# Optimization experiments

Measured on AMD Instinct MI355X. Metric: run time of the kernel, lower is better.

Reference implementation:

```python
import jax, jax.numpy as jnp
import numpy as np

N_NODES = 100000
N_EDGES = 1600000
D = 64


def setup_inputs() -> dict:
    key = jax.random.key(0)
    ks = jax.random.split(key, 9)
    x = jax.random.normal(ks[0], (N_NODES, D), dtype=jnp.float32)
    src = jax.random.randint(ks[1], (N_EDGES,), 0, N_NODES, dtype=jnp.int64)
    dst = jax.random.randint(ks[2], (N_EDGES,), 0, N_NODES, dtype=jnp.int64)
    s = 1.0 / np.sqrt(D)
    W_self1 = jax.random.normal(ks[3], (D, D), dtype=jnp.float32) * s
    W_neigh1 = jax.random.normal(ks[4], (D, D), dtype=jnp.float32) * s
    b1 = jnp.zeros((D,), dtype=jnp.float32)
    W_self2 = jax.random.normal(ks[5], (D, D), dtype=jnp.float32) * s
    W_neigh2 = jax.random.normal(ks[6], (D, D), dtype=jnp.float32) * s
    b2 = jnp.zeros((D,), dtype=jnp.float32)
    return {"x": x, "src": src, "dst": dst,
            "W_self1": W_self1, "W_neigh1": W_neigh1, "b1": b1,
            "W_self2": W_self2, "W_neigh2": W_neigh2, "b2": b2}


def _sage_layer(h, src, dst, W_self, W_neigh, b, n_nodes):
    # gather source-node features along edges: [E, d]
    msg = h[src]
    # sum messages into destination nodes, then normalize by in-degree (mean agg)
    agg = jax.ops.segment_sum(msg, dst, num_segments=n_nodes)
    deg = jax.ops.segment_sum(jnp.ones((src.shape[0], 1), h.dtype), dst,
                              num_segments=n_nodes)
    h_neigh = agg / jnp.maximum(deg, 1.0)
    # DGL SAGEConv (mean): fc_self(h) + fc_neigh(h_neigh) + bias
    return h @ W_self + h_neigh @ W_neigh + b


def reference(x, src, dst, W_self1, W_neigh1, b1, W_self2, W_neigh2, b2):
    n = x.shape[0]
    h = _sage_layer(x, src, dst, W_self1, W_neigh1, b1, n)
    # note: source module's forward applies no activation between layers
    h = _sage_layer(h, src, dst, W_self2, W_neigh2, b2, n)
    return h
```

## Files before the change

kernel.cpp:

```cpp
#include <hip/hip_runtime.h>
#include <hip/hip_bf16.h>


#define D 64
#define CAP 64
#define BNODES 256
#define BCAP 4736
#define MAXNB 512
#define WT_STRIDE 144

typedef __bf16 bf16x8 __attribute__((ext_vector_type(8)));
typedef float  f32x4  __attribute__((ext_vector_type(4)));

__device__ __forceinline__ unsigned pack2(float a, float b) {
    __hip_bfloat162 t = __float22bfloat162_rn(make_float2(a, b));
    return *(unsigned*)&t;
}
__device__ __forceinline__ unsigned short f2b(float f) {
    __hip_bfloat16 b = __float2bfloat16(f);
    return *(unsigned short*)&b;
}


__global__ void __launch_bounds__(256)
prep_kernel(const float4* __restrict__ x, uint4* __restrict__ xb4,
            unsigned* __restrict__ xsent, unsigned* __restrict__ h1sent,
            int* __restrict__ esent,
            const int* __restrict__ src, const int* __restrict__ dst,
            int* __restrict__ gcur, int* __restrict__ gbucket,
            int E, int NB, int n8, int bin_blocks, int N) {
    const int bid = blockIdx.x;
    const int t   = threadIdx.x;

    if (bid < bin_blocks) {
        __shared__ int hist[MAXNB];
        for (int i = t; i < NB; i += 256) hist[i] = 0;
        __syncthreads();

        const int e4_total = E >> 2;
        const int base4    = bid * 1024;

        int4 sv[4], dv[4];
        bool have[4];
        #pragma unroll
        for (int k = 0; k < 4; ++k) {
            int i4 = base4 + t + k * 256;
            have[k] = i4 < e4_total;
            if (have[k]) {
                sv[k] = ((const int4*)src)[i4];
                dv[k] = ((const int4*)dst)[i4];
            }
        }

        #pragma unroll
        for (int k = 0; k < 4; ++k) if (have[k]) {
            atomicAdd(&hist[dv[k].x >> 8], 1);
            atomicAdd(&hist[dv[k].y >> 8], 1);
            atomicAdd(&hist[dv[k].z >> 8], 1);
            atomicAdd(&hist[dv[k].w >> 8], 1);
        }

        int  tail_s = 0, tail_d = 0;
        bool have_tail = false;
        if (bid == 0) {
            int e = (e4_total << 2) + t;
            if (e < E) {
                tail_s = src[e]; tail_d = dst[e]; have_tail = true;
                atomicAdd(&hist[tail_d >> 8], 1);
            }
        }
        __syncthreads();

        for (int i = t; i < NB; i += 256) {
            int c = hist[i];
            hist[i] = (c > 0) ? atomicAdd(&gcur[i], c) : 0;
        }
        __syncthreads();

        #pragma unroll
        for (int k = 0; k < 4; ++k) if (have[k]) {
            int4 s = sv[k], d = dv[k];
            int b, p;
            b = d.x >> 8; p = atomicAdd(&hist[b], 1); if (p < BCAP) gbucket[b * BCAP + p] = ((d.x & 255) << 17) | s.x;
            b = d.y >> 8; p = atomicAdd(&hist[b], 1); if (p < BCAP) gbucket[b * BCAP + p] = ((d.y & 255) << 17) | s.y;
            b = d.z >> 8; p = atomicAdd(&hist[b], 1); if (p < BCAP) gbucket[b * BCAP + p] = ((d.z & 255) << 17) | s.z;
            b = d.w >> 8; p = atomicAdd(&hist[b], 1); if (p < BCAP) gbucket[b * BCAP + p] = ((d.w & 255) << 17) | s.w;
        }
        if (have_tail) {
            int b = tail_d >> 8, p = atomicAdd(&hist[b], 1);
            if (p < BCAP) gbucket[b * BCAP + p] = ((tail_d & 255) << 17) | tail_s;
        }
        return;
    }

    const int cb = bid - bin_blocks;
    const int i  = cb * 256 + t;
    if (i < n8) {
        float4 a = x[2 * i], b = x[2 * i + 1];
        uint4 o;
        o.x = pack2(a.x, a.y);
        o.y = pack2(a.z, a.w);
        o.z = pack2(b.x, b.y);
        o.w = pack2(b.z, b.w);
        xb4[i] = o;
    }
    if (cb == 0) {
        if (t < 32)              xsent[t] = 0u;
        else if (t < 64)         h1sent[t - 32] = 0u;
        else if (t < 64 + CAP)   esent[t - 64] = N;
    }
}


__global__ void __launch_bounds__(256)
ellify_kernel(const int* __restrict__ gcur, const int* __restrict__ gbucket,
              int* __restrict__ cnt, int* __restrict__ edge_idx, int N) {
    __shared__ int scnt[BNODES];
    scnt[threadIdx.x] = 0;
    __syncthreads();

    const int b     = blockIdx.x;
    const int ne    = min(gcur[b], BCAP);
    const int node0 = b << 8;

    for (int e = threadIdx.x; e < ne; e += 256) {
        int p   = gbucket[b * BCAP + e];
        int s   = p & 0x1FFFF;
        int ld  = p >> 17;
        int pos = atomicAdd(&scnt[ld], 1);
        if (pos < CAP) edge_idx[(size_t)(node0 + ld) * CAP + pos] = s;
    }
    __syncthreads();

    int node = node0 + threadIdx.x;
    if (node < N) {
        int raw = scnt[threadIdx.x];
        cnt[node] = raw;
        int c  = min(raw, CAP);
        int c8 = (c + 7) & ~7;
        for (int p = c; p < c8; ++p)
            edge_idx[(size_t)node * CAP + p] = N;
    }
}


__device__ __forceinline__ void acc8(float& a0, float& a1, float& a2, float& a3,
                                     float& a4, float& a5, float& a6, float& a7,
                                     uint4 u) {
    a0 += __uint_as_float(u.x << 16);
    a1 += __uint_as_float(u.x & 0xffff0000u);
    a2 += __uint_as_float(u.y << 16);
    a3 += __uint_as_float(u.y & 0xffff0000u);
    a4 += __uint_as_float(u.z << 16);
    a5 += __uint_as_float(u.z & 0xffff0000u);
    a6 += __uint_as_float(u.w << 16);
    a7 += __uint_as_float(u.w & 0xffff0000u);
}

__device__ __forceinline__ bf16x8 asbf(uint4 u) {
    union { uint4 a; bf16x8 v; } c; c.a = u; return c.v;
}

__global__ void __launch_bounds__(256, 3)
fused_kernel(const unsigned short* __restrict__ h,
             const int* __restrict__ cnt,
             const int* __restrict__ edge_idx,
             const float* __restrict__ Wself,
             const float* __restrict__ Wneigh,
             const float* __restrict__ bias,
             float* __restrict__ out_f32,
             unsigned short* __restrict__ out_bf16, int N) {
    __shared__ __align__(16) unsigned short wt[64 * WT_STRIDE];

    {
        const int t    = threadIdx.x;
        const int krow = t >> 1;
        const int c0   = (t & 1) * 32;
        const float* Wrow = (krow < 64) ? (Wself + krow * 64)
                                        : (Wneigh + (krow - 64) * 64);
        for (int i = 0; i < 32; i += 4) {
            float4 w = *(const float4*)(Wrow + c0 + i);
            const int n0 = c0 + i;
            wt[(n0 + 0) * WT_STRIDE + krow] = f2b(w.x);
            wt[(n0 + 1) * WT_STRIDE + krow] = f2b(w.y);
            wt[(n0 + 2) * WT_STRIDE + krow] = f2b(w.z);
            wt[(n0 + 3) * WT_STRIDE + krow] = f2b(w.w);
        }
    }
    __syncthreads();

    const int lane = threadIdx.x & 63;
    const int q    = lane & 7;
    const int g    = lane >> 3;
    const int col  = lane & 15;
    const int quad = lane >> 4;
    const int wave = blockIdx.x * (blockDim.x >> 6) + (threadIdx.x >> 6);
    const int n_waves = gridDim.x * (blockDim.x >> 6);

    const int tiles = (N + 15) >> 4;
    int t = wave;
    if (t >= tiles) return;

    float bv[4];
    #pragma unroll
    for (int nt = 0; nt < 4; ++nt) bv[nt] = bias[nt * 16 + col];

    const uint4* __restrict__ h4 = (const uint4*)h;
    const int SENT = N * CAP;

    int pcA, pcB, psrA, psrB;
    {
        const int nodeA = t * 16 + g, nodeB = nodeA + 8;
        const int aA = (nodeA < N) ? nodeA : 0;
        const int aB = (nodeB < N) ? nodeB : 0;
        const int lA = cnt[aA], lB = cnt[aB];
        pcA  = (nodeA < N) ? lA : 0;
        pcB  = (nodeB < N) ? lB : 0;
        psrA = edge_idx[aA * CAP + q];
        psrB = edge_idx[aB * CAP + q];
    }

    for (; t < tiles; t += n_waves) {
        const int cA  = min(pcA, CAP), cB = min(pcB, CAP);
        const int c8A = (cA + 7) & ~7, c8B = (cB + 7) & ~7;
        const int nodeA  = t * 16 + g;
        const int startA = ((nodeA < N) ? nodeA : 0) * CAP;
        const int startB = ((nodeA + 8 < N) ? nodeA + 8 : 0) * CAP;
        const int cmax = max(c8A, c8B);
        const int b0   = g << 3;
        int srA = psrA, srB = psrB;

        {
            const int tn = t + n_waves;
            const int tc = (tn < tiles) ? tn : t;
            const int nA = tc * 16 + g, nB = nA + 8;
            const int aA = (nA < N) ? nA : 0;
            const int aB = (nB < N) ? nB : 0;
            const int lA = cnt[aA], lB = cnt[aB];
            pcA  = (nA < N) ? lA : 0;
            pcB  = (nB < N) ? lB : 0;
            psrA = edge_idx[aA * CAP + q];
            psrB = edge_idx[aB * CAP + q];
        }

        int row = t * 16 + col;
        if (row >= N) row = N - 1;
        uint4 A0u = h4[(size_t)row * 8 + quad];
        uint4 A1u = h4[(size_t)row * 8 + 4 + quad];

        float a0 = 0.f, a1 = 0.f, a2 = 0.f, a3 = 0.f;
        float a4 = 0.f, a5 = 0.f, a6 = 0.f, a7 = 0.f;
        float b0f = 0.f, b1f = 0.f, b2f = 0.f, b3f = 0.f;
        float b4f = 0.f, b5f = 0.f, b6f = 0.f, b7f = 0.f;

        for (int j = 0; j < cmax; j += 8) {
            const int jn = j + 8;
            const int srA_n = edge_idx[((jn < c8A) ? startA + jn : SENT) + q];
            const int srB_n = edge_idx[((jn < c8B) ? startB + jn : SENT) + q];

            const int sA0 = __shfl(srA, b0 + 0, 64);
            const int sA1 = __shfl(srA, b0 + 1, 64);
            const int sA2 = __shfl(srA, b0 + 2, 64);
            const int sA3 = __shfl(srA, b0 + 3, 64);
            const int sA4 = __shfl(srA, b0 + 4, 64);
            const int sA5 = __shfl(srA, b0 + 5, 64);
            const int sA6 = __shfl(srA, b0 + 6, 64);
            const int sA7 = __shfl(srA, b0 + 7, 64);
            const int sB0 = __shfl(srB, b0 + 0, 64);
            const int sB1 = __shfl(srB, b0 + 1, 64);
            const int sB2 = __shfl(srB, b0 + 2, 64);
            const int sB3 = __shfl(srB, b0 + 3, 64);
            const int sB4 = __shfl(srB, b0 + 4, 64);
            const int sB5 = __shfl(srB, b0 + 5, 64);
            const int sB6 = __shfl(srB, b0 + 6, 64);
            const int sB7 = __shfl(srB, b0 + 7, 64);

            uint4 uA0 = h4[(size_t)sA0 * 8 + q];
            uint4 uA1 = h4[(size_t)sA1 * 8 + q];
            uint4 uA2 = h4[(size_t)sA2 * 8 + q];
            uint4 uA3 = h4[(size_t)sA3 * 8 + q];
            uint4 uA4 = h4[(size_t)sA4 * 8 + q];
            uint4 uA5 = h4[(size_t)sA5 * 8 + q];
            uint4 uA6 = h4[(size_t)sA6 * 8 + q];
            uint4 uA7 = h4[(size_t)sA7 * 8 + q];
            uint4 uB0 = h4[(size_t)sB0 * 8 + q];
            uint4 uB1 = h4[(size_t)sB1 * 8 + q];
            uint4 uB2 = h4[(size_t)sB2 * 8 + q];
            uint4 uB3 = h4[(size_t)sB3 * 8 + q];
            uint4 uB4 = h4[(size_t)sB4 * 8 + q];
            uint4 uB5 = h4[(size_t)sB5 * 8 + q];
            uint4 uB6 = h4[(size_t)sB6 * 8 + q];
            uint4 uB7 = h4[(size_t)sB7 * 8 + q];

            __builtin_amdgcn_sched_barrier(0);

            acc8(a0, a1, a2, a3, a4, a5, a6, a7, uA0);
            acc8(a0, a1, a2, a3, a4, a5, a6, a7, uA1);
            acc8(a0, a1, a2, a3, a4, a5, a6, a7, uA2);
            acc8(a0, a1, a2, a3, a4, a5, a6, a7, uA3);
            acc8(a0, a1, a2, a3, a4, a5, a6, a7, uA4);
            acc8(a0, a1, a2, a3, a4, a5, a6, a7, uA5);
            acc8(a0, a1, a2, a3, a4, a5, a6, a7, uA6);
            acc8(a0, a1, a2, a3, a4, a5, a6, a7, uA7);
            acc8(b0f, b1f, b2f, b3f, b4f, b5f, b6f, b7f, uB0);
            acc8(b0f, b1f, b2f, b3f, b4f, b5f, b6f, b7f, uB1);
            acc8(b0f, b1f, b2f, b3f, b4f, b5f, b6f, b7f, uB2);
            acc8(b0f, b1f, b2f, b3f, b4f, b5f, b6f, b7f, uB3);
            acc8(b0f, b1f, b2f, b3f, b4f, b5f, b6f, b7f, uB4);
            acc8(b0f, b1f, b2f, b3f, b4f, b5f, b6f, b7f, uB5);
            acc8(b0f, b1f, b2f, b3f, b4f, b5f, b6f, b7f, uB6);
            acc8(b0f, b1f, b2f, b3f, b4f, b5f, b6f, b7f, uB7);

            srA = srA_n;
            srB = srB_n;
        }

        const float invA = (cA > 0) ? 1.0f / (float)cA : 0.0f;
        const float invB = (cB > 0) ? 1.0f / (float)cB : 0.0f;
        uint4 P0, P1;
        P0.x = pack2(a0 * invA, a1 * invA);
        P0.y = pack2(a2 * invA, a3 * invA);
        P0.z = pack2(a4 * invA, a5 * invA);
        P0.w = pack2(a6 * invA, a7 * invA);
        P1.x = pack2(b0f * invB, b1f * invB);
        P1.y = pack2(b2f * invB, b3f * invB);
        P1.z = pack2(b4f * invB, b5f * invB);
        P1.w = pack2(b6f * invB, b7f * invB);

        const int srcA2 = ((lane & 7) << 3) + quad;
        const int srcA3 = srcA2 + 4;
        const bool hi   = (lane & 8) != 0;
        uint4 A2u, A3u;
        {
            unsigned l0 = __shfl(P0.x, srcA2, 64), h0 = __shfl(P1.x, srcA2, 64);
            unsigned l1 = __shfl(P0.y, srcA2, 64), h1 = __shfl(P1.y, srcA2, 64);
            unsigned l2 = __shfl(P0.z, srcA2, 64), h2 = __shfl(P1.z, srcA2, 64);
            unsigned l3 = __shfl(P0.w, srcA2, 64), h3 = __shfl(P1.w, srcA2, 64);
            A2u.x = hi ? h0 : l0;  A2u.y = hi ? h1 : l1;
            A2u.z = hi ? h2 : l2;  A2u.w = hi ? h3 : l3;
        }
        {
            unsigned l0 = __shfl(P0.x, srcA3, 64), h0 = __shfl(P1.x, srcA3, 64);
            unsigned l1 = __shfl(P0.y, srcA3, 64), h1 = __shfl(P1.y, srcA3, 64);
            unsigned l2 = __shfl(P0.z, srcA3, 64), h2 = __shfl(P1.z, srcA3, 64);
            unsigned l3 = __shfl(P0.w, srcA3, 64), h3 = __shfl(P1.w, srcA3, 64);
            A3u.x = hi ? h0 : l0;  A3u.y = hi ? h1 : l1;
            A3u.z = hi ? h2 : l2;  A3u.w = hi ? h3 : l3;
        }

        bf16x8 A0 = asbf(A0u), A1 = asbf(A1u);
        bf16x8 A2 = asbf(A2u), A3 = asbf(A3u);

        __builtin_amdgcn_sched_barrier(0);
        int ob = 0;
        asm volatile("" : "+v"(ob));
        bf16x8 Bf[4][4];
        #pragma unroll
        for (int nt = 0; nt < 4; ++nt) {
            const int n = nt * 16 + col;
            #pragma unroll
            for (int kk = 0; kk < 4; ++kk) {
                const int kcat0 = ((kk >= 2) ? 64 : 0) + (kk & 1) * 32 + quad * 8;
                const char* p = (const char*)wt + n * (WT_STRIDE * 2) + kcat0 * 2 + ob;
                Bf[nt][kk] = *(const bf16x8*)p;
            }
        }

        #pragma unroll
        for (int nt = 0; nt < 4; ++nt) {
            f32x4 acc = {bv[nt], bv[nt], bv[nt], bv[nt]};
            acc = __builtin_amdgcn_mfma_f32_16x16x32_bf16(A0, Bf[nt][0], acc, 0, 0, 0);
            acc = __builtin_amdgcn_mfma_f32_16x16x32_bf16(A1, Bf[nt][1], acc, 0, 0, 0);
            acc = __builtin_amdgcn_mfma_f32_16x16x32_bf16(A2, Bf[nt][2], acc, 0, 0, 0);
            acc = __builtin_amdgcn_mfma_f32_16x16x32_bf16(A3, Bf[nt][3], acc, 0, 0, 0);
            if (out_f32) {
                #pragma unroll
                for (int r = 0; r < 4; ++r) {
                    const int orow = t * 16 + quad * 4 + r;
                    if (orow < N) out_f32[(size_t)orow * D + nt * 16 + col] = acc[r];
                }
            } else {
                #pragma unroll
                for (int r = 0; r < 4; ++r) {
                    const int orow = t * 16 + quad * 4 + r;
                    if (orow < N) out_bf16[(size_t)orow * D + nt * 16 + col] = f2b(acc[r]);
                }
            }
        }
    }
}


extern "C" void kernel_launch(void* const* d_in, const int* in_sizes, int n_in,
                              void* d_out, int out_size, void* d_ws, size_t ws_size,
                              hipStream_t stream) {
    const float* x   = (const float*)d_in[0];
    const int*   src = (const int*)d_in[1];
    const int*   dst = (const int*)d_in[2];
    const float* Ws1 = (const float*)d_in[3];
    const float* Wn1 = (const float*)d_in[4];
    const float* b1  = (const float*)d_in[5];
    const float* Ws2 = (const float*)d_in[6];
    const float* Wn2 = (const float*)d_in[7];
    const float* b2  = (const float*)d_in[8];

    const int N = in_sizes[0] / D;
    const int E = in_sizes[1];

    float* out = (float*)d_out;

    const int NB = (N + BNODES - 1) / BNODES;

    int* gcur      = (int*)d_ws;
    int* cnt       = gcur + 512;
    int* edge_idx  = cnt + N;
    unsigned short* xb   = (unsigned short*)(edge_idx + (size_t)(N + 1) * CAP);
    unsigned short* h1b  = xb + (size_t)(N + 1) * D;
    int* gbucket   = (int*)(h1b + (size_t)(N + 1) * D);

    const int n8         = N * D / 8;
    const int cvt_blocks = (n8 + 255) / 256;
    const int e4_total   = E >> 2;
    const int bin_blocks = (e4_total + 1023) / 1024 > 0 ? (e4_total + 1023) / 1024 : 1;

    hipMemsetAsync(gcur, 0, 512 * sizeof(int), stream);

    prep_kernel<<<bin_blocks + cvt_blocks, 256, 0, stream>>>(
        (const float4*)x, (uint4*)xb,
        (unsigned*)(xb + (size_t)N * D), (unsigned*)(h1b + (size_t)N * D),
        edge_idx + (size_t)N * CAP,
        src, dst, gcur, gbucket, E, NB, n8, bin_blocks, N);

    ellify_kernel<<<NB, 256, 0, stream>>>(gcur, gbucket, cnt, edge_idx, N);

    const int fblocks = 768;

    fused_kernel<<<fblocks, 256, 0, stream>>>(xb, cnt, edge_idx, Ws1, Wn1, b1,
                                              nullptr, h1b, N);
    fused_kernel<<<fblocks, 256, 0, stream>>>(h1b, cnt, edge_idx, Ws2, Wn2, b2,
                                              out, nullptr, N);
}
```

Measured before the change: 197.7 us.

## Sort edges locally in shared memory before coalesced global bucket and ELL writes

The binning kernel now computes a per-block prefix sum over bucket counts, counting-sorts its edges into shared memory, and then writes each bucket's entries to global memory as contiguous runs instead of scattering them individually. The ellify kernel likewise counting-sorts each bucket by local node in shared memory and writes full 64-entry ELL rows with vectorized int4 stores, padding with the sentinel. The aim is coalesced global writes in place of random 4-byte scatters. In exchange it adds serial single-thread prefix scans, more shared memory (which may lower occupancy), and extra barriers, and every row is now written in full.

```diff
diff --git a/kernel.cpp b/kernel.cpp
--- a/kernel.cpp
+++ b/kernel.cpp
@@ -33,8 +33,14 @@
     const int t   = threadIdx.x;
 
     if (bid < bin_blocks) {
-        __shared__ int hist[MAXNB];
-        for (int i = t; i < NB; i += 256) hist[i] = 0;
+        __shared__ int            bcnt[MAXNB];
+        __shared__ int            pofs[MAXNB];
+        __shared__ int            sofs[MAXNB];
+        __shared__ int            gbase[MAXNB];
+        __shared__ int            ssort[4096];
+        __shared__ unsigned short sbkt[4096];
+
+        for (int i = t; i < NB; i += 256) bcnt[i] = 0;
         __syncthreads();
 
         const int e4_total = E >> 2;
@@ -54,41 +60,53 @@
 
         #pragma unroll
         for (int k = 0; k < 4; ++k) if (have[k]) {
-            atomicAdd(&hist[dv[k].x >> 8], 1);
-            atomicAdd(&hist[dv[k].y >> 8], 1);
-            atomicAdd(&hist[dv[k].z >> 8], 1);
-            atomicAdd(&hist[dv[k].w >> 8], 1);
-        }
-
-        int  tail_s = 0, tail_d = 0;
-        bool have_tail = false;
+            atomicAdd(&bcnt[dv[k].x >> 8], 1);
+            atomicAdd(&bcnt[dv[k].y >> 8], 1);
+            atomicAdd(&bcnt[dv[k].z >> 8], 1);
+            atomicAdd(&bcnt[dv[k].w >> 8], 1);
+        }
+        __syncthreads();
+
+        if (t == 0) {
+            int acc = 0;
+            for (int i = 0; i < NB; ++i) { pofs[i] = acc; acc += bcnt[i]; }
+        }
+        __syncthreads();
+        for (int i = t; i < NB; i += 256) sofs[i] = pofs[i];
+        __syncthreads();
+
+        #pragma unroll
+        for (int k = 0; k < 4; ++k) if (have[k]) {
+            int4 s = sv[k], d = dv[k];
+            int b, p;
+            b = d.x >> 8; p = atomicAdd(&sofs[b], 1); ssort[p] = ((d.x & 255) << 17) | s.x; sbkt[p] = (unsigned short)b;
+            b = d.y >> 8; p = atomicAdd(&sofs[b], 1); ssort[p] = ((d.y & 255) << 17) | s.y; sbkt[p] = (unsigned short)b;
+            b = d.z >> 8; p = atomicAdd(&sofs[b], 1); ssort[p] = ((d.z & 255) << 17) | s.z; sbkt[p] = (unsigned short)b;
+            b = d.w >> 8; p = atomicAdd(&sofs[b], 1); ssort[p] = ((d.w & 255) << 17) | s.w; sbkt[p] = (unsigned short)b;
+        }
+        __syncthreads();
+
+        for (int i = t; i < NB; i += 256) {
+            int c = bcnt[i];
+            gbase[i] = (c > 0) ? atomicAdd(&gcur[i], c) : 0;
+        }
+        __syncthreads();
+
+        const int eblk = (min(base4 + 1024, e4_total) - base4) << 2;
+        for (int i = t; i < eblk; i += 256) {
+            const int b    = sbkt[i];
+            const int gpos = gbase[b] + (i - pofs[b]);
+            if (gpos < BCAP) gbucket[b * BCAP + gpos] = ssort[i];
+        }
+
         if (bid == 0) {
             int e = (e4_total << 2) + t;
             if (e < E) {
-                tail_s = src[e]; tail_d = dst[e]; have_tail = true;
-                atomicAdd(&hist[tail_d >> 8], 1);
+                int s = src[e], d = dst[e];
+                int b = d >> 8;
+                int p = atomicAdd(&gcur[b], 1);
+                if (p < BCAP) gbucket[b * BCAP + p] = ((d & 255) << 17) | s;
             }
-        }
-        __syncthreads();
-
-        for (int i = t; i < NB; i += 256) {
-            int c = hist[i];
-            hist[i] = (c > 0) ? atomicAdd(&gcur[i], c) : 0;
-        }
-        __syncthreads();
-
-        #pragma unroll
-        for (int k = 0; k < 4; ++k) if (have[k]) {
-            int4 s = sv[k], d = dv[k];
-            int b, p;
-            b = d.x >> 8; p = atomicAdd(&hist[b], 1); if (p < BCAP) gbucket[b * BCAP + p] = ((d.x & 255) << 17) | s.x;
-            b = d.y >> 8; p = atomicAdd(&hist[b], 1); if (p < BCAP) gbucket[b * BCAP + p] = ((d.y & 255) << 17) | s.y;
-            b = d.z >> 8; p = atomicAdd(&hist[b], 1); if (p < BCAP) gbucket[b * BCAP + p] = ((d.z & 255) << 17) | s.z;
-            b = d.w >> 8; p = atomicAdd(&hist[b], 1); if (p < BCAP) gbucket[b * BCAP + p] = ((d.w & 255) << 17) | s.w;
-        }
-        if (have_tail) {
-            int b = tail_d >> 8, p = atomicAdd(&hist[b], 1);
-            if (p < BCAP) gbucket[b * BCAP + p] = ((tail_d & 255) << 17) | tail_s;
         }
         return;
     }
@@ -115,31 +133,62 @@
 __global__ void __launch_bounds__(256)
 ellify_kernel(const int* __restrict__ gcur, const int* __restrict__ gbucket,
               int* __restrict__ cnt, int* __restrict__ edge_idx, int N) {
-    __shared__ int scnt[BNODES];
-    scnt[threadIdx.x] = 0;
+    __shared__ int sval[BCAP];
+    __shared__ int ncnt[BNODES], nst[BNODES], nofs[BNODES];
+
+    const int t = threadIdx.x;
+    ncnt[t] = 0;
     __syncthreads();
 
     const int b     = blockIdx.x;
     const int ne    = min(gcur[b], BCAP);
     const int node0 = b << 8;
 
-    for (int e = threadIdx.x; e < ne; e += 256) {
+    for (int e = t; e < ne; e += 256) {
+        int p = gbucket[b * BCAP + e];
+        atomicAdd(&ncnt[p >> 17], 1);
+    }
+    __syncthreads();
+
+    if (t == 0) {
+        int acc = 0;
+        for (int i = 0; i < BNODES; ++i) { nst[i] = acc; acc += ncnt[i]; }
+    }
+    __syncthreads();
+    nofs[t] = nst[t];
+    __syncthreads();
+
+    for (int e = t; e < ne; e += 256) {
         int p   = gbucket[b * BCAP + e];
-        int s   = p & 0x1FFFF;
         int ld  = p >> 17;
-        int pos = atomicAdd(&scnt[ld], 1);
-        if (pos < CAP) edge_idx[(size_t)(node0 + ld) * CAP + pos] = s;
-    }
-    __syncthreads();
-
-    int node = node0 + threadIdx.x;
-    if (node < N) {
-        int raw = scnt[threadIdx.x];
-        cnt[node] = raw;
-        int c  = min(raw, CAP);
-        int c8 = (c + 7) & ~7;
-        for (int p = c; p < c8; ++p)
-            edge_idx[(size_t)node * CAP + p] = N;
+        int pos = atomicAdd(&nofs[ld], 1);
+        sval[pos] = p & 0x1FFFF;
+    }
+    __syncthreads();
+
+    {
+        int node = node0 + t;
+        if (node < N) cnt[node] = ncnt[t];
+    }
+
+    const int qq = t & 7;
+    for (int base = (t >> 3); base < BNODES; base += 32) {
+        const int node = node0 + base;
+        if (node >= N) continue;
+        const int c  = min(ncnt[base], CAP);
+        const int st = nst[base];
+        int4* rowp = (int4*)(edge_idx + (size_t)node * CAP);
+        #pragma unroll
+        for (int half = 0; half < 2; ++half) {
+            const int slot = qq + half * 8;
+            const int k0   = slot * 4;
+            int4 v;
+            v.x = (k0 + 0 < c) ? sval[st + k0 + 0] : N;
+            v.y = (k0 + 1 < c) ? sval[st + k0 + 1] : N;
+            v.z = (k0 + 2 < c) ? sval[st + k0 + 2] : N;
+            v.w = (k0 + 3 < c) ? sval[st + k0 + 3] : N;
+            rowp[slot] = v;
+        }
     }
 }
 
```

Result: no change. 195.6 us (-1.1%).
